# Performance work log

Hardware: AMD Instinct MI355X
Metric: run time of the kernel (lower is better)

## Reference

```python
import jax, jax.numpy as jnp
import numpy as np

B, T, C, HS = 8, 2048, 1024, 64


def setup_inputs() -> dict:
    key = jax.random.key(0)
    ks = jax.random.split(key, 4)
    x = jax.random.normal(ks[0], (B, T, C), dtype=jnp.float32)
    Wq = jax.random.normal(ks[1], (C, HS), dtype=jnp.float32) * (C ** -0.5)
    Wk = jax.random.normal(ks[2], (C, HS), dtype=jnp.float32) * (C ** -0.5)
    Wv = jax.random.normal(ks[3], (C, HS), dtype=jnp.float32) * (C ** -0.5)
    mask = jnp.tril(jnp.ones((T, T), dtype=jnp.int32))  # causal mask
    return {"x": x, "mask": mask, "Wq": Wq, "Wk": Wk, "Wv": Wv}


def reference(x, mask, Wq, Wk, Wv):
    # x: [B,T,C]; bias-free projections to head_size
    q = jnp.einsum("btc,ch->bth", x, Wq)
    k = jnp.einsum("btc,ch->bth", x, Wk)
    v = jnp.einsum("btc,ch->bth", x, Wv)
    # NOTE: original scales by C**-0.5 (n_embd), not head_size**-0.5
    wei = jnp.einsum("bth,bsh->bts", q, k) * (x.shape[-1] ** -0.5)
    wei = jnp.where(mask[None, :, :] == 0, -jnp.inf, wei)
    wei = jax.nn.softmax(wei, axis=-1)
    # dropout is identity in eval / p=0
    out = jnp.einsum("bts,bsh->bth", wei, v)
    return out
```

## Files before the change

### kernel.cpp

```cpp
#include <hip/hip_runtime.h>
#include <hip/hip_bf16.h>


#define B_  8
#define T_  2048
#define C_  1024
#define HS_ 64
#define MROWS (B_ * T_)

typedef __attribute__((ext_vector_type(8))) short bf16x8;
typedef __attribute__((ext_vector_type(4))) float f32x4;
typedef __attribute__((ext_vector_type(4))) float float4v;

#define SCALE_LOG2 0.04508422037445829f

__device__ __forceinline__ short f2bs(float f) {
    __hip_bfloat16 h = __float2bfloat16(f);
    short s;
    __builtin_memcpy(&s, &h, 2);
    return s;
}

__global__ __launch_bounds__(256) void wt_kernel(
    const float* __restrict__ Wq,
    const float* __restrict__ Wk,
    const float* __restrict__ Wv,
    __hip_bfloat16* __restrict__ Wt) {
    __shared__ float tile[64][65];
    const int m  = blockIdx.x >> 4;
    const int r0 = (blockIdx.x & 15) * 64;
    const float* W = (m == 0) ? Wq : (m == 1) ? Wk : Wv;
    const int i = threadIdx.x >> 6;
    const int j = threadIdx.x & 63;
#pragma unroll
    for (int p = 0; p < 16; ++p) {
        int r = p * 4 + i;
        tile[r][j] = W[(size_t)(r0 + r) * HS_ + j];
    }
    __syncthreads();
#pragma unroll
    for (int p = 0; p < 16; ++p) {
        int h = p * 4 + i;
        Wt[(size_t)m * (HS_ * C_) + (size_t)h * C_ + r0 + j] =
            __float2bfloat16(tile[j][h]);
    }
}

__global__ __launch_bounds__(256, 2) void proj_kernel(
    const float* __restrict__ x,
    const __hip_bfloat16* __restrict__ Wt,
    __hip_bfloat16* __restrict__ Q,
    __hip_bfloat16* __restrict__ Kp,
    __hip_bfloat16* __restrict__ Vt)
{
    __shared__ float xt0[32 * 68];
    __shared__ float xt1[32 * 68];

    const int lane = threadIdx.x & 63;
    const int wave = threadIdx.x >> 6;
    const int quad = lane >> 4;
    const int l15  = lane & 15;
    const int row0 = blockIdx.x * 32;

    const float* gsrc[8];
#pragma unroll
    for (int rr = 0; rr < 8; ++rr)
        gsrc[rr] = x + (size_t)(row0 + wave * 8 + rr) * C_ + lane;

    const __hip_bfloat16* wbase[3];
#pragma unroll
    for (int j = 0; j < 3; ++j) {
        int nt = wave * 3 + j;
        int h  = ((nt & 3) * 16) + l15;
        wbase[j] = Wt + (size_t)(nt >> 2) * (HS_ * C_) + (size_t)h * C_ + quad * 8;
    }

    f32x4 acc[2][3];
#pragma unroll
    for (int rt = 0; rt < 2; ++rt)
#pragma unroll
        for (int j = 0; j < 3; ++j)
            acc[rt][j] = (f32x4){0.f, 0.f, 0.f, 0.f};

    bf16x8 bfr0[2][3], bfr1[2][3];

#define ISSUE_DMA(XT, kc)                                                    \
    do {                                                                     \
        _Pragma("unroll")                                                    \
        for (int rr = 0; rr < 8; ++rr)                                       \
            __builtin_amdgcn_global_load_lds(                                \
                (const __attribute__((address_space(1))) unsigned*)          \
                    (gsrc[rr] + (kc)),                                       \
                (__attribute__((address_space(3))) unsigned*)                \
                    (&XT[(wave * 8 + rr) * 68]),                             \
                4, 0, 0);                                                    \
    } while (0)

#define LOAD_B(BF, kc)                                                       \
    do {                                                                     \
        _Pragma("unroll")                                                    \
        for (int ks = 0; ks < 2; ++ks)                                       \
            _Pragma("unroll")                                                \
            for (int j = 0; j < 3; ++j)                                      \
                BF[ks][j] = *(const bf16x8*)(wbase[j] + (kc) + ks * 32);     \
    } while (0)

#define COMPUTE(XT, BF)                                                      \
    do {                                                                     \
        _Pragma("unroll")                                                    \
        for (int ks = 0; ks < 2; ++ks) {                                     \
            bf16x8 a[2];                                                     \
            _Pragma("unroll")                                                \
            for (int rt = 0; rt < 2; ++rt) {                                 \
                const float4v* p = (const float4v*)                          \
                    &XT[(rt * 16 + l15) * 68 + ks * 32 + quad * 8];          \
                float4v f0 = p[0], f1 = p[1];                                \
                _Pragma("unroll")                                            \
                for (int e = 0; e < 4; ++e) {                                \
                    a[rt][e]     = f2bs(f0[e]);                              \
                    a[rt][4 + e] = f2bs(f1[e]);                              \
                }                                                            \
            }                                                                \
            _Pragma("unroll")                                                \
            for (int rt = 0; rt < 2; ++rt)                                   \
                _Pragma("unroll")                                            \
                for (int j = 0; j < 3; ++j)                                  \
                    acc[rt][j] = __builtin_amdgcn_mfma_f32_16x16x32_bf16(    \
                        a[rt], BF[ks][j], acc[rt][j], 0, 0, 0);              \
        }                                                                    \
    } while (0)

    ISSUE_DMA(xt0, 0);
    LOAD_B(bfr0, 0);

#pragma unroll 1
    for (int kc = 0; kc < C_; kc += 128) {
        __syncthreads();
        if (kc + 64 < C_) {
            ISSUE_DMA(xt1, kc + 64);
            LOAD_B(bfr1, kc + 64);
        }
        COMPUTE(xt0, bfr0);
        __syncthreads();
        if (kc + 128 < C_) {
            ISSUE_DMA(xt0, kc + 128);
            LOAD_B(bfr0, kc + 128);
        }
        COMPUTE(xt1, bfr1);
    }
#undef ISSUE_DMA
#undef LOAD_B
#undef COMPUTE

#pragma unroll
    for (int rt = 0; rt < 2; ++rt) {
#pragma unroll
        for (int j = 0; j < 3; ++j) {
            int nt  = wave * 3 + j;
            int mtx = nt >> 2;
            int col = (nt & 3) * 16 + l15;
#pragma unroll
            for (int r = 0; r < 4; ++r) {
                int row = row0 + rt * 16 + quad * 4 + r;
                __hip_bfloat16 v = __float2bfloat16(acc[rt][j][r]);
                if (mtx == 0) {
                    Q[(size_t)row * HS_ + col] = v;
                } else if (mtx == 1) {
                    Kp[(size_t)row * HS_ + col] = v;
                } else {
                    int bidx = row >> 11;
                    int t    = row & 2047;
                    Vt[((size_t)bidx * HS_ + col) * T_ + t] = v;
                }
            }
        }
    }
}

__global__ __launch_bounds__(256, 2) void attn_kernel(
    const __hip_bfloat16* __restrict__ Q,
    const __hip_bfloat16* __restrict__ Kp,
    const __hip_bfloat16* __restrict__ Vt,
    float* __restrict__ out)
{
    __shared__ __align__(16) __hip_bfloat16 plds[4][16 * 64];
    __shared__ float o_lds[4][16][64];
    __shared__ float l_lds[4][16][16];

    const int tid  = threadIdx.x;
    const int wv   = tid >> 6;
    const int lane = tid & 63;
    const int quad = lane >> 4;
    const int l15  = lane & 15;
    const int b    = blockIdx.x & 7;
    const int lt   = 127 - (blockIdx.x >> 3);
    const int qb   = lt * 16;
    const int rowg = b * T_ + qb;

    bf16x8 qf0 = *(const bf16x8*)(Q + (size_t)(rowg + l15) * HS_ + quad * 8);
    bf16x8 qf1 = *(const bf16x8*)(Q + (size_t)(rowg + l15) * HS_ + 32 + quad * 8);

    f32x4 o[4];
#pragma unroll
    for (int j = 0; j < 4; ++j) o[j] = (f32x4){0.f, 0.f, 0.f, 0.f};
    float lp[4] = {0.f, 0.f, 0.f, 0.f};

    __hip_bfloat16* pb = plds[wv];
    const int nt = (qb + 15) / 64 + 1;

#define LOADKV(KF, VF, kb_)                                                  \
    do {                                                                     \
        const __hip_bfloat16* Kb_ = Kp + (size_t)(b * T_ + (kb_)) * HS_;     \
        _Pragma("unroll")                                                    \
        for (int c = 0; c < 4; ++c)                                          \
            _Pragma("unroll")                                                \
            for (int h = 0; h < 2; ++h)                                      \
                KF[c][h] = *(const bf16x8*)                                  \
                    (Kb_ + (size_t)(c * 16 + l15) * HS_ + h * 32 + quad * 8);\
        _Pragma("unroll")                                                    \
        for (int h = 0; h < 2; ++h)                                          \
            _Pragma("unroll")                                                \
            for (int j = 0; j < 4; ++j)                                      \
                VF[h][j] = *(const bf16x8*)                                  \
                    (Vt + ((size_t)b * HS_ + j * 16 + l15) * T_ +            \
                     (kb_) + h * 32 + quad * 8);                             \
    } while (0)

#define PROC(KF, VF, kb_)                                                    \
    do {                                                                     \
        f32x4 s[4];                                                          \
        _Pragma("unroll")                                                    \
        for (int c = 0; c < 4; ++c) {                                        \
            s[c] = (f32x4){0.f, 0.f, 0.f, 0.f};                              \
            s[c] = __builtin_amdgcn_mfma_f32_16x16x32_bf16(                  \
                qf0, KF[c][0], s[c], 0, 0, 0);                               \
            s[c] = __builtin_amdgcn_mfma_f32_16x16x32_bf16(                  \
                qf1, KF[c][1], s[c], 0, 0, 0);                               \
        }                                                                    \
        const bool msk = ((kb_) + 63 > qb);                                  \
        float p[4][4];                                                       \
        _Pragma("unroll")                                                    \
        for (int c = 0; c < 4; ++c)                                          \
            _Pragma("unroll")                                                \
            for (int r = 0; r < 4; ++r) {                                    \
                p[c][r] = exp2f(s[c][r] * SCALE_LOG2);                       \
                if (msk) {                                                   \
                    int row = qb + quad * 4 + r;                             \
                    if ((kb_) + c * 16 + l15 > row) p[c][r] = 0.f;           \
                }                                                            \
                lp[r] += p[c][r];                                            \
            }                                                                \
        _Pragma("unroll")                                                    \
        for (int r = 0; r < 4; ++r)                                          \
            _Pragma("unroll")                                                \
            for (int c = 0; c < 4; ++c)                                      \
                pb[(quad * 4 + r) * 64 + c * 16 + l15] =                     \
                    __float2bfloat16(p[c][r]);                               \
        asm volatile("s_waitcnt lgkmcnt(0)" ::: "memory");                   \
        bf16x8 pf0 = *(const bf16x8*)(pb + l15 * 64 + quad * 8);             \
        bf16x8 pf1 = *(const bf16x8*)(pb + l15 * 64 + 32 + quad * 8);        \
        _Pragma("unroll")                                                    \
        for (int j = 0; j < 4; ++j) {                                        \
            o[j] = __builtin_amdgcn_mfma_f32_16x16x32_bf16(                  \
                pf0, VF[0][j], o[j], 0, 0, 0);                               \
            o[j] = __builtin_amdgcn_mfma_f32_16x16x32_bf16(                  \
                pf1, VF[1][j], o[j], 0, 0, 0);                               \
        }                                                                    \
    } while (0)

    bf16x8 kA[4][2], vA[2][4], kB[4][2], vB[2][4];
    if (wv < nt) LOADKV(kA, vA, wv * 64);
    int i = 0;
#pragma unroll 1
    for (; wv + 4 * (i + 1) < nt; i += 2) {
        LOADKV(kB, vB, (wv + 4 * (i + 1)) * 64);
        PROC(kA, vA, (wv + 4 * i) * 64);
        if (wv + 4 * (i + 2) < nt) LOADKV(kA, vA, (wv + 4 * (i + 2)) * 64);
        PROC(kB, vB, (wv + 4 * (i + 1)) * 64);
    }
    if (wv + 4 * i < nt) PROC(kA, vA, (wv + 4 * i) * 64);
#undef LOADKV
#undef PROC

#pragma unroll
    for (int j = 0; j < 4; ++j)
#pragma unroll
        for (int r = 0; r < 4; ++r)
            o_lds[wv][quad * 4 + r][j * 16 + l15] = o[j][r];
#pragma unroll
    for (int r = 0; r < 4; ++r)
        l_lds[wv][quad * 4 + r][l15] = lp[r];
    __syncthreads();

    if (tid < 16) {
        float s = 0.f;
#pragma unroll
        for (int w = 0; w < 4; ++w)
            for (int c = 0; c < 16; ++c) s += l_lds[w][tid][c];
        l_lds[0][tid][0] = 1.0f / s;
    }
    __syncthreads();

    const int h = tid & 63;
#pragma unroll
    for (int k = 0; k < 4; ++k) {
        int row = (tid >> 6) * 4 + k;
        float s = o_lds[0][row][h] + o_lds[1][row][h] +
                  o_lds[2][row][h] + o_lds[3][row][h];
        out[(size_t)(rowg + row) * HS_ + h] = s * l_lds[0][row][0];
    }
}

extern "C" void kernel_launch(void* const* d_in, const int* in_sizes, int n_in,
                              void* d_out, int out_size, void* d_ws, size_t ws_size,
                              hipStream_t stream) {
    (void)in_sizes; (void)n_in; (void)out_size; (void)ws_size;
    const float* x  = (const float*)d_in[0];
    const float* Wq = (const float*)d_in[2];
    const float* Wk = (const float*)d_in[3];
    const float* Wv = (const float*)d_in[4];

    __hip_bfloat16* ws = (__hip_bfloat16*)d_ws;
    __hip_bfloat16* Wt = ws;
    __hip_bfloat16* Q  = ws + 196608;
    __hip_bfloat16* Kp = ws + 196608 + 1048576;
    __hip_bfloat16* Vt = ws + 196608 + 2 * 1048576;

    wt_kernel<<<48, 256, 0, stream>>>(Wq, Wk, Wv, Wt);
    proj_kernel<<<MROWS / 32, 256, 0, stream>>>(x, Wt, Q, Kp, Vt);
    attn_kernel<<<(T_ / 16) * B_, 256, 0, stream>>>(Q, Kp, Vt, (float*)d_out);
}
```

Measured before the change: 163.2 us.

## Process 32 query rows per attention block to reuse K/V tiles

Each attention block now covers 32 query rows (two 16-row MFMA tiles) instead of 16, so every K and V fragment loaded from global memory feeds twice as many MFMAs and the grid shrinks by half. V loads move inside the processing step and are no longer double-buffered, which cuts register pressure from the doubled Q/O/accumulator state. The trade-off is fewer blocks for occupancy and load balance on the causal triangle, more LDS per block, and V load latency that is now exposed instead of prefetched.

```diff
diff --git a/kernel.cpp b/kernel.cpp
--- a/kernel.cpp
+++ b/kernel.cpp
@@ -183,9 +183,9 @@
     const __hip_bfloat16* __restrict__ Vt,
     float* __restrict__ out)
 {
-    __shared__ __align__(16) __hip_bfloat16 plds[4][16 * 64];
-    __shared__ float o_lds[4][16][64];
-    __shared__ float l_lds[4][16][16];
+    __shared__ __align__(16) __hip_bfloat16 plds[4][32 * 64];
+    __shared__ float o_lds[4][32][64];
+    __shared__ float l_lds[4][32][16];
 
     const int tid  = threadIdx.x;
     const int wv   = tid >> 6;
@@ -193,22 +193,29 @@
     const int quad = lane >> 4;
     const int l15  = lane & 15;
     const int b    = blockIdx.x & 7;
-    const int lt   = 127 - (blockIdx.x >> 3);
-    const int qb   = lt * 16;
+    const int lt   = 63 - (blockIdx.x >> 3);
+    const int qb   = lt * 32;
     const int rowg = b * T_ + qb;
 
-    bf16x8 qf0 = *(const bf16x8*)(Q + (size_t)(rowg + l15) * HS_ + quad * 8);
-    bf16x8 qf1 = *(const bf16x8*)(Q + (size_t)(rowg + l15) * HS_ + 32 + quad * 8);
-
-    f32x4 o[4];
-#pragma unroll
-    for (int j = 0; j < 4; ++j) o[j] = (f32x4){0.f, 0.f, 0.f, 0.f};
-    float lp[4] = {0.f, 0.f, 0.f, 0.f};
+    bf16x8 qf[2][2];
+#pragma unroll
+    for (int rt = 0; rt < 2; ++rt)
+#pragma unroll
+        for (int h = 0; h < 2; ++h)
+            qf[rt][h] = *(const bf16x8*)
+                (Q + (size_t)(rowg + rt * 16 + l15) * HS_ + h * 32 + quad * 8);
+
+    f32x4 o[2][4];
+#pragma unroll
+    for (int rt = 0; rt < 2; ++rt)
+#pragma unroll
+        for (int j = 0; j < 4; ++j) o[rt][j] = (f32x4){0.f, 0.f, 0.f, 0.f};
+    float lp[2][4] = {{0.f,0.f,0.f,0.f},{0.f,0.f,0.f,0.f}};
 
     __hip_bfloat16* pb = plds[wv];
-    const int nt = (qb + 15) / 64 + 1;
-
-#define LOADKV(KF, VF, kb_)                                                  \
+    const int nt = (qb + 31) / 64 + 1;
+
+#define LOADK(KF, kb_)                                                       \
     do {                                                                     \
         const __hip_bfloat16* Kb_ = Kp + (size_t)(b * T_ + (kb_)) * HS_;     \
         _Pragma("unroll")                                                    \
@@ -217,82 +224,90 @@
             for (int h = 0; h < 2; ++h)                                      \
                 KF[c][h] = *(const bf16x8*)                                  \
                     (Kb_ + (size_t)(c * 16 + l15) * HS_ + h * 32 + quad * 8);\
+    } while (0)
+
+#define PROC(KF, kb_)                                                        \
+    do {                                                                     \
+        bf16x8 vf[2][4];                                                     \
         _Pragma("unroll")                                                    \
         for (int h = 0; h < 2; ++h)                                          \
             _Pragma("unroll")                                                \
             for (int j = 0; j < 4; ++j)                                      \
-                VF[h][j] = *(const bf16x8*)                                  \
+                vf[h][j] = *(const bf16x8*)                                  \
                     (Vt + ((size_t)b * HS_ + j * 16 + l15) * T_ +            \
                      (kb_) + h * 32 + quad * 8);                             \
-    } while (0)
-
-#define PROC(KF, VF, kb_)                                                    \
-    do {                                                                     \
-        f32x4 s[4];                                                          \
-        _Pragma("unroll")                                                    \
-        for (int c = 0; c < 4; ++c) {                                        \
-            s[c] = (f32x4){0.f, 0.f, 0.f, 0.f};                              \
-            s[c] = __builtin_amdgcn_mfma_f32_16x16x32_bf16(                  \
-                qf0, KF[c][0], s[c], 0, 0, 0);                               \
-            s[c] = __builtin_amdgcn_mfma_f32_16x16x32_bf16(                  \
-                qf1, KF[c][1], s[c], 0, 0, 0);                               \
+        f32x4 s[2][4];                                                       \
+        _Pragma("unroll")                                                    \
+        for (int rt = 0; rt < 2; ++rt)                                       \
+            _Pragma("unroll")                                                \
+            for (int c = 0; c < 4; ++c) {                                    \
+                s[rt][c] = (f32x4){0.f, 0.f, 0.f, 0.f};                      \
+                s[rt][c] = __builtin_amdgcn_mfma_f32_16x16x32_bf16(          \
+                    qf[rt][0], KF[c][0], s[rt][c], 0, 0, 0);                 \
+                s[rt][c] = __builtin_amdgcn_mfma_f32_16x16x32_bf16(          \
+                    qf[rt][1], KF[c][1], s[rt][c], 0, 0, 0);                 \
+            }                                                                \
+        const bool msk = ((kb_) + 63 > qb);                                  \
+        _Pragma("unroll")                                                    \
+        for (int rt = 0; rt < 2; ++rt)                                       \
+            _Pragma("unroll")                                                \
+            for (int c = 0; c < 4; ++c)                                      \
+                _Pragma("unroll")                                            \
+                for (int r = 0; r < 4; ++r) {                                \
+                    float pv = exp2f(s[rt][c][r] * SCALE_LOG2);              \
+                    if (msk) {                                               \
+                        int row = qb + rt * 16 + quad * 4 + r;               \
+                        if ((kb_) + c * 16 + l15 > row) pv = 0.f;            \
+                    }                                                        \
+                    lp[rt][r] += pv;                                         \
+                    pb[(rt * 16 + quad * 4 + r) * 64 + c * 16 + l15] =       \
+                        __float2bfloat16(pv);                                \
+                }                                                            \
+        asm volatile("s_waitcnt lgkmcnt(0)" ::: "memory");                   \
+        _Pragma("unroll")                                                    \
+        for (int rt = 0; rt < 2; ++rt) {                                     \
+            bf16x8 pf0 = *(const bf16x8*)                                    \
+                (pb + (rt * 16 + l15) * 64 + quad * 8);                      \
+            bf16x8 pf1 = *(const bf16x8*)                                    \
+                (pb + (rt * 16 + l15) * 64 + 32 + quad * 8);                 \
+            _Pragma("unroll")                                                \
+            for (int j = 0; j < 4; ++j) {                                    \
+                o[rt][j] = __builtin_amdgcn_mfma_f32_16x16x32_bf16(          \
+                    pf0, vf[0][j], o[rt][j], 0, 0, 0);                       \
+                o[rt][j] = __builtin_amdgcn_mfma_f32_16x16x32_bf16(          \
+                    pf1, vf[1][j], o[rt][j], 0, 0, 0);                       \
+            }                                                                \
         }                                                                    \
-        const bool msk = ((kb_) + 63 > qb);                                  \
-        float p[4][4];                                                       \
-        _Pragma("unroll")                                                    \
-        for (int c = 0; c < 4; ++c)                                          \
-            _Pragma("unroll")                                                \
-            for (int r = 0; r < 4; ++r) {                                    \
-                p[c][r] = exp2f(s[c][r] * SCALE_LOG2);                       \
-                if (msk) {                                                   \
-                    int row = qb + quad * 4 + r;                             \
-                    if ((kb_) + c * 16 + l15 > row) p[c][r] = 0.f;           \
-                }                                                            \
-                lp[r] += p[c][r];                                            \
-            }                                                                \
-        _Pragma("unroll")                                                    \
-        for (int r = 0; r < 4; ++r)                                          \
-            _Pragma("unroll")                                                \
-            for (int c = 0; c < 4; ++c)                                      \
-                pb[(quad * 4 + r) * 64 + c * 16 + l15] =                     \
-                    __float2bfloat16(p[c][r]);                               \
-        asm volatile("s_waitcnt lgkmcnt(0)" ::: "memory");                   \
-        bf16x8 pf0 = *(const bf16x8*)(pb + l15 * 64 + quad * 8);             \
-        bf16x8 pf1 = *(const bf16x8*)(pb + l15 * 64 + 32 + quad * 8);        \
-        _Pragma("unroll")                                                    \
-        for (int j = 0; j < 4; ++j) {                                        \
-            o[j] = __builtin_amdgcn_mfma_f32_16x16x32_bf16(                  \
-                pf0, VF[0][j], o[j], 0, 0, 0);                               \
-            o[j] = __builtin_amdgcn_mfma_f32_16x16x32_bf16(                  \
-                pf1, VF[1][j], o[j], 0, 0, 0);                               \
-        }                                                                    \
-    } while (0)
-
-    bf16x8 kA[4][2], vA[2][4], kB[4][2], vB[2][4];
-    if (wv < nt) LOADKV(kA, vA, wv * 64);
+    } while (0)
+
+    bf16x8 kA[4][2], kB[4][2];
+    if (wv < nt) LOADK(kA, wv * 64);
     int i = 0;
 #pragma unroll 1
     for (; wv + 4 * (i + 1) < nt; i += 2) {
-        LOADKV(kB, vB, (wv + 4 * (i + 1)) * 64);
-        PROC(kA, vA, (wv + 4 * i) * 64);
-        if (wv + 4 * (i + 2) < nt) LOADKV(kA, vA, (wv + 4 * (i + 2)) * 64);
-        PROC(kB, vB, (wv + 4 * (i + 1)) * 64);
-    }
-    if (wv + 4 * i < nt) PROC(kA, vA, (wv + 4 * i) * 64);
-#undef LOADKV
+        LOADK(kB, (wv + 4 * (i + 1)) * 64);
+        PROC(kA, (wv + 4 * i) * 64);
+        if (wv + 4 * (i + 2) < nt) LOADK(kA, (wv + 4 * (i + 2)) * 64);
+        PROC(kB, (wv + 4 * (i + 1)) * 64);
+    }
+    if (wv + 4 * i < nt) PROC(kA, (wv + 4 * i) * 64);
+#undef LOADK
 #undef PROC
 
 #pragma unroll
-    for (int j = 0; j < 4; ++j)
+    for (int rt = 0; rt < 2; ++rt) {
+#pragma unroll
+        for (int j = 0; j < 4; ++j)
+#pragma unroll
+            for (int r = 0; r < 4; ++r)
+                o_lds[wv][rt * 16 + quad * 4 + r][j * 16 + l15] = o[rt][j][r];
 #pragma unroll
         for (int r = 0; r < 4; ++r)
-            o_lds[wv][quad * 4 + r][j * 16 + l15] = o[j][r];
-#pragma unroll
-    for (int r = 0; r < 4; ++r)
-        l_lds[wv][quad * 4 + r][l15] = lp[r];
+            l_lds[wv][rt * 16 + quad * 4 + r][l15] = lp[rt][r];
+    }
     __syncthreads();
 
-    if (tid < 16) {
+    if (tid < 32) {
         float s = 0.f;
 #pragma unroll
         for (int w = 0; w < 4; ++w)
@@ -303,8 +318,8 @@
 
     const int h = tid & 63;
 #pragma unroll
-    for (int k = 0; k < 4; ++k) {
-        int row = (tid >> 6) * 4 + k;
+    for (int k = 0; k < 8; ++k) {
+        int row = (tid >> 6) * 8 + k;
         float s = o_lds[0][row][h] + o_lds[1][row][h] +
                   o_lds[2][row][h] + o_lds[3][row][h];
         out[(size_t)(rowg + row) * HS_ + h] = s * l_lds[0][row][0];
@@ -328,5 +343,5 @@
 
     wt_kernel<<<48, 256, 0, stream>>>(Wq, Wk, Wv, Wt);
     proj_kernel<<<MROWS / 32, 256, 0, stream>>>(x, Wt, Q, Kp, Vt);
-    attn_kernel<<<(T_ / 16) * B_, 256, 0, stream>>>(Q, Kp, Vt, (float*)d_out);
-}
+    attn_kernel<<<(T_ / 32) * B_, 256, 0, stream>>>(Q, Kp, Vt, (float*)d_out);
+}
```

After: 154.6 us. 5.3% less time.
